# Optimization experiments

Hardware: AMD Instinct MI355X
Metric: run time of the kernel (lower is better)

Reference implementation:

```python
import jax, jax.numpy as jnp
import numpy as np

BINS = 6  # torch.histc(bins=6, min=0, max=256) in rarity()


def _border_mask(h, w, dtype):
    m = jnp.ones((h, w), dtype)
    return m.at[0, :].set(0).at[-1, :].set(0).at[:, 0].set(0).at[:, -1].set(0)


def _norm(x, lo, hi, axes):
    # normalize_tensor: map to [lo,hi]; all-zeros if constant map
    mn = x.min(axes, keepdims=True)
    mx = x.max(axes, keepdims=True)
    d = mx - mn
    ds = jnp.where(d == 0, jnp.ones_like(d), d)
    out = (x - mn) / ds * (hi - lo) + lo
    return jnp.where(d == 0, jnp.zeros_like(out), out)


def _ponder(x, axes):
    # map_ponderation: normalize to [0,1] then scale by (max-mean)^2
    w = (x.max(axes, keepdims=True) - x.mean(axes, keepdims=True)) ** 2
    return _norm(x, 0.0, 1.0, axes) * w


def _rarity_all(ch):
    # Vectorized rarity() over all channels. ch: [C,H,W]
    C, H, W = ch.shape
    ch = ch * _border_mask(H, W, ch.dtype)          # zero 1-px border
    ch = _norm(ch, 0.0, 256.0, (1, 2))              # per-channel -> [0,256]
    # torch.histc over [0,256]: bin = floor(v*bins/256), max value in last bin
    bin_idx = jnp.clip((ch * (BINS / 256.0)).astype(jnp.int32), 0, BINS - 1)
    hist = jax.nn.one_hot(bin_idx, BINS, dtype=ch.dtype).sum((1, 2))  # [C,BINS]
    hist = hist / hist.sum(-1, keepdims=True)
    hist = -jnp.log(hist + 1e-4)
    # lookup: (channel*bins - 1).long().clamp(0, bins-1)  (channel in [0,256], as in source)
    lut_idx = jnp.clip((ch * BINS - 1).astype(jnp.int32), 0, BINS - 1)
    dst = hist[jnp.arange(C)[:, None, None], lut_idx]  # [C,H,W] rarity lookup
    dst = _norm(dst, 0.0, 1.0, (1, 2))
    return _ponder(dst, (1, 2))


def _apply_rarity(x):
    # x: [1,C,H,W] -> [H,W]
    ch = x[0]
    H, W = ch.shape[-2:]
    r = _rarity_all(ch)
    # channel 0: ponderated again, no extra border zeroing (as in source)
    p0 = _ponder(r[0], (0, 1))
    rest = r[1:] * _border_mask(H, W, r.dtype)  # channels 1..C-1: border zeroed
    p = p0 + _ponder(rest, (1, 2)).sum(0)
    return _norm(p, 0.0, 1.0, (0, 1))  # threshold=None -> no thresholding


def _resize240(m):
    # T.Resize((240,240), bilinear) ~ half-pixel linear resize
    return jax.image.resize(m, (240, 240), method='linear')


def _forward(layers):
    # group layers into packs by spatial resolution (static, shapes known)
    packs = {}
    for t in layers:
        packs.setdefault(t.shape[-2:], []).append(t)
    group_maps = []
    for pack in packs.values():
        maps = [_resize240(_apply_rarity(t)) for t in pack]
        fused = maps[0] * 0.0
        for m in maps:  # fuse_itti
            fused = fused + _ponder(m, (0, 1))
        group_maps.append(_norm(fused, 0.0, 256.0, (0, 1)))
    groups = jnp.stack(group_maps, -1)  # [240,240,n_packs]
    return groups.sum(-1), groups


def setup_inputs() -> dict:
    key = jax.random.key(0)
    shapes = ([(1, 64, 224, 224)] * 2 + [(1, 128, 112, 112)] * 2 +
              [(1, 256, 56, 56)] * 3 + [(1, 512, 28, 28)] * 3 +
              [(1, 512, 14, 14)] * 3)
    keys = jax.random.split(key, len(shapes))
    return {f"x{i}": jax.random.uniform(keys[i], s, jnp.float32)
            for i, s in enumerate(shapes)}


def reference(x0, x1, x2, x3, x4, x5, x6, x7, x8, x9, x10, x11, x12):
    return _forward([x0, x1, x2, x3, x4, x5, x6, x7, x8, x9, x10, x11, x12])
```

## Files before the change

kernel.cpp:

```cpp
#include <hip/hip_runtime.h>
#include <math.h>

#define NT 13
#define RHW 57600
#define PIXB 8192

struct Meta {
  const float* x[NT];
  int C[NT];
  int H[NT];
  float hsc[NT];
  int chanOff[NT + 1];
  int pixOff[NT + 1];
  int mmOff[NT + 1];
  int nchMM[NT];
  int pmOff[NT + 1];
  int npcPM[NT];
  int pcOff[NT + 1];
};

__device__ __forceinline__ unsigned encf(float f) {
  unsigned u = __float_as_uint(f);
  return (u & 0x80000000u) ? ~u : (u | 0x80000000u);
}
__device__ __forceinline__ float decf(unsigned e) {
  unsigned u = (e & 0x80000000u) ? (e & 0x7fffffffu) : ~e;
  return __uint_as_float(u);
}

__device__ __forceinline__ int segOf(const int* off, int b) {
  int t = 0;
  while (t + 1 < NT && b >= off[t + 1]) t++;
  return t;
}

__global__ __launch_bounds__(256) void k_init(unsigned* cstats, unsigned* hist,
                                              unsigned long long* pq, int co, int po) {
  int i = blockIdx.x * 256 + threadIdx.x;
  int stride = gridDim.x * 256;
  for (int k = i; k < po; k += stride) pq[k] = 0ull;
  for (int k = i; k < 12 * co; k += stride) hist[k] = 0u;
  for (int k = i; k < co; k += stride) { cstats[2 * k] = 0xFFFFFFFFu; cstats[2 * k + 1] = 0u; }
}

template <int HH>
__device__ __forceinline__ void mm_body(const float* __restrict__ ch, int pix0, int pix1, float& mn, float& mx) {
  constexpr int W = HH, H = HH;
  int i40 = pix0 >> 2, i41 = pix1 >> 2;
  for (int i4 = i40 + (int)threadIdx.x; i4 < i41; i4 += 256) {
    float4 v = reinterpret_cast<const float4*>(ch)[i4];
#pragma unroll
    for (int j = 0; j < 4; j++) {
      int idx = i4 * 4 + j;
      int h = idx / W, w = idx - h * W;
      bool ok = h > 0 && h < (H - 1) && w > 0 && w < (W - 1);
      float f = (j == 0) ? v.x : (j == 1) ? v.y : (j == 2) ? v.z : v.w;
      if (ok) { mn = fminf(mn, f); mx = fmaxf(mx, f); }
    }
  }
}

__global__ __launch_bounds__(256) void k_minmax(Meta m, unsigned* cstats) {
  int b = blockIdx.x;
  int t = segOf(m.mmOff, b);
  int local = b - m.mmOff[t];
  int nch = m.nchMM[t];
  int c = local / nch, k = local - c * nch;
  int HW = m.H[t] * m.H[t];
  const float* ch = m.x[t] + (size_t)c * HW;
  int pix0 = k * PIXB, pix1 = min(pix0 + PIXB, HW);
  float mn = INFINITY, mx = -INFINITY;
  switch (m.H[t]) {
    case 224: mm_body<224>(ch, pix0, pix1, mn, mx); break;
    case 112: mm_body<112>(ch, pix0, pix1, mn, mx); break;
    case 56:  mm_body<56>(ch, pix0, pix1, mn, mx); break;
    case 28:  mm_body<28>(ch, pix0, pix1, mn, mx); break;
    default:  mm_body<14>(ch, pix0, pix1, mn, mx); break;
  }
#pragma unroll
  for (int o = 32; o > 0; o >>= 1) {
    mn = fminf(mn, __shfl_down(mn, o));
    mx = fmaxf(mx, __shfl_down(mx, o));
  }
  __shared__ float smn[4], smx[4];
  int wid = threadIdx.x >> 6;
  if ((threadIdx.x & 63) == 0) { smn[wid] = mn; smx[wid] = mx; }
  __syncthreads();
  if (threadIdx.x == 0) {
    for (int i = 1; i < 4; i++) { mn = fminf(mn, smn[i]); mx = fmaxf(mx, smx[i]); }
    int g = m.chanOff[t] + c;
    atomicMin(&cstats[2 * g], encf(mn));
    atomicMax(&cstats[2 * g + 1], encf(mx));
  }
}

template <int HH>
__device__ __forceinline__ void hist_body(const float* __restrict__ ch, int pix0, int pix1,
                                          float mn, float invd, unsigned* sh) {
  constexpr int W = HH, H = HH;
  int i40 = pix0 >> 2, i41 = pix1 >> 2;
  int nIter = (i41 - i40 + 255) >> 8;
  int lane = threadIdx.x & 63;
  unsigned cnt = 0;
  for (int it = 0; it < nIter; ++it) {
    int i4 = i40 + it * 256 + (int)threadIdx.x;
    bool valid = i4 < i41;
    float4 v = make_float4(0.f, 0.f, 0.f, 0.f);
    if (valid) v = reinterpret_cast<const float4*>(ch)[i4];
    int code[8];
#pragma unroll
    for (int j = 0; j < 4; j++) {
      int idx = i4 * 4 + j;
      int h = idx / W, w = idx - h * W;
      bool ok = valid && h > 0 && h < (H - 1) && w > 0 && w < (W - 1);
      float f = (j == 0) ? v.x : (j == 1) ? v.y : (j == 2) ? v.z : v.w;
      float vv = (f - mn) * invd * 256.0f;
      int bin = (int)(vv * 0.0234375f);
      bin = bin < 0 ? 0 : (bin > 5 ? 5 : bin);
      float tt = vv * 6.0f - 1.0f;
      int li = (int)tt;
      li = li < 0 ? 0 : (li > 5 ? 5 : li);
      code[j] = ok ? bin : -1;
      code[4 + j] = ok ? li : -1;
    }
#pragma unroll
    for (int j = 0; j < 4; j++) {
#pragma unroll
      for (int q = 0; q < 6; q++) {
        unsigned long long mb = __ballot(code[j] == q);
        if (lane == q) cnt += (unsigned)__popcll(mb);
        unsigned long long ml = __ballot(code[4 + j] == q);
        if (lane == 6 + q) cnt += (unsigned)__popcll(ml);
      }
    }
  }
  if (lane < 12) atomicAdd(&sh[lane], cnt);
}

__global__ __launch_bounds__(256) void k_hist(Meta m, const unsigned* cstats, unsigned* hist) {
  int b = blockIdx.x;
  int t = segOf(m.mmOff, b);
  int local = b - m.mmOff[t];
  int nch = m.nchMM[t];
  int c = local / nch, k = local - c * nch;
  int HW = m.H[t] * m.H[t];
  const float* ch = m.x[t] + (size_t)c * HW;
  int g = m.chanOff[t] + c;
  float mn = fminf(decf(cstats[2 * g]), 0.f);
  float mx = fmaxf(decf(cstats[2 * g + 1]), 0.f);
  float d = mx - mn;
  float invd = d > 0.f ? 1.0f / d : 0.f;
  int pix0 = k * PIXB, pix1 = min(pix0 + PIXB, HW);
  __shared__ unsigned sh[12];
  if (threadIdx.x < 12) sh[threadIdx.x] = 0;
  __syncthreads();
  switch (m.H[t]) {
    case 224: hist_body<224>(ch, pix0, pix1, mn, invd, sh); break;
    case 112: hist_body<112>(ch, pix0, pix1, mn, invd, sh); break;
    case 56:  hist_body<56>(ch, pix0, pix1, mn, invd, sh); break;
    case 28:  hist_body<28>(ch, pix0, pix1, mn, invd, sh); break;
    default:  hist_body<14>(ch, pix0, pix1, mn, invd, sh); break;
  }
  __syncthreads();
  if (threadIdx.x < 12) atomicAdd(&hist[12 * g + threadIdx.x], sh[threadIdx.x]);
}

__global__ void k_lut(Meta m, const unsigned* cstats, const unsigned* hist, float* lutg, int nch) {
  int b = blockIdx.x * blockDim.x + threadIdx.x;
  if (b >= nch) return;
  int t = segOf(m.chanOff, b);
  int cl = b - m.chanOff[t];
  int H = m.H[t], W = m.H[t], HW = H * W;
  float fHW = (float)HW;
  int nb = 2 * (H + W) - 4;
  float mn = fminf(decf(cstats[2 * b]), 0.f);
  float mx = fmaxf(decf(cstats[2 * b + 1]), 0.f);
  float d = mx - mn;
  float invd = d > 0.f ? 1.0f / d : 0.f;
  float vb = (0.f - mn) * invd * 256.0f;
  int bin_b = (int)(vb * 0.0234375f);
  bin_b = bin_b < 0 ? 0 : (bin_b > 5 ? 5 : bin_b);
  float ttb = vb * 6.0f - 1.0f;
  int lib = (int)ttb;
  lib = lib < 0 ? 0 : (lib > 5 ? 5 : lib);
  unsigned hh[12];
  for (int j = 0; j < 12; j++) hh[j] = hist[12 * b + j];
  hh[bin_b] += (unsigned)nb;
  hh[6 + lib] += (unsigned)nb;
  float hl[6];
  for (int j = 0; j < 6; j++) hl[j] = -logf((float)hh[j] / fHW + 1e-4f);
  float mn2 = INFINITY, mx2 = -INFINITY, sum2 = 0.f;
  for (int j = 0; j < 6; j++) {
    unsigned cc = hh[6 + j];
    if (cc) { mn2 = fminf(mn2, hl[j]); mx2 = fmaxf(mx2, hl[j]); sum2 += (float)cc * hl[j]; }
  }
  float d2 = mx2 - mn2;
  float RL[6];
  if (d2 > 0.f) {
    float meanN = (sum2 / fHW - mn2) / d2;
    float w = 1.0f - meanN; w *= w;
    for (int j = 0; j < 6; j++) RL[j] = (hl[j] - mn2) / d2 * w;
  } else {
    for (int j = 0; j < 6; j++) RL[j] = 0.f;
  }
  float LUT[7];
  if (cl == 0) {
    float mnr = INFINITY, mxr = -INFINITY, sumr = 0.f;
    for (int j = 0; j < 6; j++) {
      unsigned cc = hh[6 + j];
      if (cc) { mnr = fminf(mnr, RL[j]); mxr = fmaxf(mxr, RL[j]); sumr += (float)cc * RL[j]; }
    }
    float dr = mxr - mnr;
    if (dr > 0.f) {
      float meanr = sumr / fHW;
      float wp = mxr - meanr; wp *= wp;
      for (int j = 0; j < 6; j++) LUT[j] = (RL[j] - mnr) / dr * wp;
      LUT[6] = LUT[lib];
    } else {
      for (int j = 0; j < 7; j++) LUT[j] = 0.f;
    }
  } else {
    float mnr = 0.f, mxr = 0.f, sumr = 0.f;
    for (int j = 0; j < 6; j++) {
      int cc = (int)hh[6 + j] - (j == lib ? nb : 0);
      if (cc > 0) { mnr = fminf(mnr, RL[j]); mxr = fmaxf(mxr, RL[j]); sumr += (float)cc * RL[j]; }
    }
    float dr = mxr - mnr;
    if (dr > 0.f) {
      float meanr = sumr / fHW;
      float wp = mxr - meanr; wp *= wp;
      for (int j = 0; j < 6; j++) LUT[j] = (RL[j] - mnr) / dr * wp;
      LUT[6] = (0.f - mnr) / dr * wp;
    } else {
      for (int j = 0; j < 7; j++) LUT[j] = 0.f;
    }
  }
  float* o = lutg + (size_t)b * 9;
  for (int j = 0; j < 7; j++) o[j] = LUT[j];
  o[7] = mn; o[8] = invd;
}

#define CCH 32
template <int HH>
__device__ __forceinline__ void pm_body(const float* __restrict__ X, int cbase, int ncb, int i4lo, int i4hi,
                                        const float* sLut, const float* sMn, const float* sInv,
                                        unsigned long long* __restrict__ Q) {
  constexpr int W = HH, H = HH;
  constexpr int HW = H * W;
  int i4 = i4lo + (int)threadIdx.x;
  if (i4 >= i4hi) return;
  int base = i4 * 4;
  int b0, b1, b2, b3;
  { int idx = base + 0; int h = idx / W, w = idx - h * W; b0 = (h == 0 || h == H - 1 || w == 0 || w == W - 1); }
  { int idx = base + 1; int h = idx / W, w = idx - h * W; b1 = (h == 0 || h == H - 1 || w == 0 || w == W - 1); }
  { int idx = base + 2; int h = idx / W, w = idx - h * W; b2 = (h == 0 || h == H - 1 || w == 0 || w == W - 1); }
  { int idx = base + 3; int h = idx / W, w = idx - h * W; b3 = (h == 0 || h == H - 1 || w == 0 || w == W - 1); }
  float a0 = 0.f, a1 = 0.f, a2 = 0.f, a3 = 0.f;
  const float4* Xp = reinterpret_cast<const float4*>(X + (size_t)cbase * HW);
#pragma unroll 4
  for (int cl = 0; cl < ncb; ++cl) {
    float4 v = Xp[(size_t)cl * (HW / 4) + i4];
    float mnc = sMn[cl], ivc = sInv[cl];
    const float* L = sLut + cl * 8;
    { float vv = (v.x - mnc) * ivc * 256.0f; float tt = vv * 6.0f - 1.0f; int li = (int)tt; li = li < 0 ? 0 : (li > 5 ? 5 : li); a0 += L[b0 ? 6 : li]; }
    { float vv = (v.y - mnc) * ivc * 256.0f; float tt = vv * 6.0f - 1.0f; int li = (int)tt; li = li < 0 ? 0 : (li > 5 ? 5 : li); a1 += L[b1 ? 6 : li]; }
    { float vv = (v.z - mnc) * ivc * 256.0f; float tt = vv * 6.0f - 1.0f; int li = (int)tt; li = li < 0 ? 0 : (li > 5 ? 5 : li); a2 += L[b2 ? 6 : li]; }
    { float vv = (v.w - mnc) * ivc * 256.0f; float tt = vv * 6.0f - 1.0f; int li = (int)tt; li = li < 0 ? 0 : (li > 5 ? 5 : li); a3 += L[b3 ? 6 : li]; }
  }
  atomicAdd(&Q[base + 0], (unsigned long long)((double)a0 * 4294967296.0));
  atomicAdd(&Q[base + 1], (unsigned long long)((double)a1 * 4294967296.0));
  atomicAdd(&Q[base + 2], (unsigned long long)((double)a2 * 4294967296.0));
  atomicAdd(&Q[base + 3], (unsigned long long)((double)a3 * 4294967296.0));
}

__global__ __launch_bounds__(256) void k_pmapQ(Meta m, const float* lutg, unsigned long long* pmapsQ) {
  __shared__ float sLut[CCH * 8];
  __shared__ float sMn[CCH];
  __shared__ float sInv[CCH];
  int b = blockIdx.x;
  int t = segOf(m.pmOff, b);
  int local = b - m.pmOff[t];
  int npc = m.npcPM[t];
  int cc = local / npc, pc = local - cc * npc;
  int C = m.C[t], HW = m.H[t] * m.H[t];
  int cbase = cc * CCH;
  int ncb = min(CCH, C - cbase);
  for (int i = threadIdx.x; i < ncb; i += 256) {
    const float* L = lutg + (size_t)(m.chanOff[t] + cbase + i) * 9;
#pragma unroll
    for (int j = 0; j < 7; j++) sLut[i * 8 + j] = L[j];
    sLut[i * 8 + 7] = 0.f;
    sMn[i] = L[7]; sInv[i] = L[8];
  }
  __syncthreads();
  int i4lo = pc * 256;
  int i4hi = min(i4lo + 256, HW >> 2);
  unsigned long long* Q = pmapsQ + m.pixOff[t];
  switch (m.H[t]) {
    case 224: pm_body<224>(m.x[t], cbase, ncb, i4lo, i4hi, sLut, sMn, sInv, Q); break;
    case 112: pm_body<112>(m.x[t], cbase, ncb, i4lo, i4hi, sLut, sMn, sInv, Q); break;
    case 56:  pm_body<56>(m.x[t], cbase, ncb, i4lo, i4hi, sLut, sMn, sInv, Q); break;
    case 28:  pm_body<28>(m.x[t], cbase, ncb, i4lo, i4hi, sLut, sMn, sInv, Q); break;
    default:  pm_body<14>(m.x[t], cbase, ncb, i4lo, i4hi, sLut, sMn, sInv, Q); break;
  }
}

__global__ __launch_bounds__(256) void k_pconv(Meta m, const unsigned long long* pmapsQ, float* pmaps, float* ppart) {
  int b = blockIdx.x;
  int t = segOf(m.pcOff, b);
  int HW = m.H[t] * m.H[t];
  int chunk = b - m.pcOff[t];
  int i4 = chunk * 256 + (int)threadIdx.x;
  float mn = INFINITY, mx = -INFINITY;
  if (i4 < (HW >> 2)) {
    size_t off = (size_t)m.pixOff[t] + (size_t)i4 * 4;
    const double inv = 1.0 / 4294967296.0;
    float4 f;
    f.x = (float)((double)pmapsQ[off + 0] * inv);
    f.y = (float)((double)pmapsQ[off + 1] * inv);
    f.z = (float)((double)pmapsQ[off + 2] * inv);
    f.w = (float)((double)pmapsQ[off + 3] * inv);
    *reinterpret_cast<float4*>(pmaps + off) = f;
    mn = fminf(fminf(f.x, f.y), fminf(f.z, f.w));
    mx = fmaxf(fmaxf(f.x, f.y), fmaxf(f.z, f.w));
  }
#pragma unroll
  for (int o = 32; o > 0; o >>= 1) {
    mn = fminf(mn, __shfl_down(mn, o));
    mx = fmaxf(mx, __shfl_down(mx, o));
  }
  __shared__ float smn[4], smx[4];
  int wid = threadIdx.x >> 6;
  if ((threadIdx.x & 63) == 0) { smn[wid] = mn; smx[wid] = mx; }
  __syncthreads();
  if (threadIdx.x == 0) {
    for (int i = 1; i < 4; i++) { mn = fminf(mn, smn[i]); mx = fmaxf(mx, smx[i]); }
    ppart[2 * b] = mn; ppart[2 * b + 1] = mx;
  }
}

__global__ __launch_bounds__(256) void k_resize(Meta m, const float* pmaps, const float* ppart,
                                                float* mmaps, float* rpart) {
  __shared__ float sMnT, sInvT;
  int t = blockIdx.x / 225;
  int blk = blockIdx.x % 225;
  int wid = threadIdx.x >> 6, lane = threadIdx.x & 63;
  if (wid == 0) {
    int n = m.pcOff[t + 1] - m.pcOff[t];
    const float* pp = ppart + (size_t)m.pcOff[t] * 2;
    float mn = INFINITY, mx = -INFINITY;
    if (lane < n) { mn = pp[2 * lane]; mx = pp[2 * lane + 1]; }
#pragma unroll
    for (int o = 32; o > 0; o >>= 1) {
      mn = fminf(mn, __shfl_down(mn, o));
      mx = fmaxf(mx, __shfl_down(mx, o));
    }
    if (lane == 0) {
      float d = mx - mn;
      sMnT = mn; sInvT = d > 0.f ? 1.0f / d : 0.f;
    }
  }
  __syncthreads();
  int pix = blk * 256 + threadIdx.x;
  int H = m.H[t], W = m.H[t];
  const float* p = pmaps + m.pixOff[t];
  float mn = sMnT, a = sInvT;
  int oy = pix / 240, ox = pix - oy * 240;
  float hs = m.hsc[t];
  float sy = ((float)oy + 0.5f) * hs - 0.5f;
  float sx = ((float)ox + 0.5f) * hs - 0.5f;
  float fy0 = floorf(sy), fx0 = floorf(sx);
  float fy = sy - fy0, fx = sx - fx0;
  int iy0 = (int)fy0, ix0 = (int)fx0;
  int y0 = iy0 < 0 ? 0 : (iy0 > H - 1 ? H - 1 : iy0);
  int y1 = iy0 + 1 < 0 ? 0 : (iy0 + 1 > H - 1 ? H - 1 : iy0 + 1);
  int x0 = ix0 < 0 ? 0 : (ix0 > W - 1 ? W - 1 : ix0);
  int x1 = ix0 + 1 < 0 ? 0 : (ix0 + 1 > W - 1 ? W - 1 : ix0 + 1);
  float v00 = p[y0 * W + x0], v01 = p[y0 * W + x1];
  float v10 = p[y1 * W + x0], v11 = p[y1 * W + x1];
  float r = (1.f - fy) * ((1.f - fx) * v00 + fx * v01) + fy * ((1.f - fx) * v10 + fx * v11);
  float mv = (r - mn) * a;
  mmaps[(size_t)t * RHW + pix] = mv;
  float bmn = mv, bmx = mv, bsm = mv;
#pragma unroll
  for (int o = 32; o > 0; o >>= 1) {
    bmn = fminf(bmn, __shfl_down(bmn, o));
    bmx = fmaxf(bmx, __shfl_down(bmx, o));
    bsm += __shfl_down(bsm, o);
  }
  __shared__ float smn[4], smx[4], ssm[4];
  if ((threadIdx.x & 63) == 0) { smn[wid] = bmn; smx[wid] = bmx; ssm[wid] = bsm; }
  __syncthreads();
  if (threadIdx.x == 0) {
    for (int i = 1; i < 4; i++) { bmn = fminf(bmn, smn[i]); bmx = fmaxf(bmx, smx[i]); bsm += ssm[i]; }
    float* rp = rpart + ((size_t)t * 225 + blk) * 3;
    rp[0] = bmn; rp[1] = bmx; rp[2] = bsm;
  }
}

__global__ __launch_bounds__(256) void k_fuse(const float* mmaps, const float* rpart,
                                              float* fusedm, float* fpart) {
  __shared__ float sMn[3], sD[3], sW[3];
  int g = blockIdx.x / 225;
  int blk = blockIdx.x % 225;
  const int gs[6] = {0, 2, 4, 7, 10, 13};
  int nt = gs[g + 1] - gs[g];
  int wid = threadIdx.x >> 6, lane = threadIdx.x & 63;
  if (wid < nt) {
    int t = gs[g] + wid;
    const float* rp = rpart + (size_t)t * 225 * 3;
    float mn = INFINITY, mx = -INFINITY, sm = 0.f;
    for (int i = lane; i < 225; i += 64) {
      mn = fminf(mn, rp[3 * i]); mx = fmaxf(mx, rp[3 * i + 1]); sm += rp[3 * i + 2];
    }
#pragma unroll
    for (int o = 32; o > 0; o >>= 1) {
      mn = fminf(mn, __shfl_down(mn, o));
      mx = fmaxf(mx, __shfl_down(mx, o));
      sm += __shfl_down(sm, o);
    }
    if (lane == 0) {
      float d = mx - mn;
      if (d > 0.f) {
        float mean = sm * (1.0f / 57600.0f);
        float w = mx - mean; w *= w;
        sMn[wid] = mn; sD[wid] = d; sW[wid] = w;
      } else {
        sMn[wid] = 0.f; sD[wid] = 0.f; sW[wid] = 0.f;
      }
    }
  }
  __syncthreads();
  int pix = blk * 256 + threadIdx.x;
  float acc = 0.f;
  for (int k = 0; k < nt; k++) {
    int t = gs[g] + k;
    if (sD[k] > 0.f) acc += (mmaps[(size_t)t * RHW + pix] - sMn[k]) / sD[k] * sW[k];
  }
  fusedm[(size_t)g * RHW + pix] = acc;
  float bmn = acc, bmx = acc;
#pragma unroll
  for (int o = 32; o > 0; o >>= 1) {
    bmn = fminf(bmn, __shfl_down(bmn, o));
    bmx = fmaxf(bmx, __shfl_down(bmx, o));
  }
  __shared__ float smn[4], smx[4];
  if ((threadIdx.x & 63) == 0) { smn[wid] = bmn; smx[wid] = bmx; }
  __syncthreads();
  if (threadIdx.x == 0) {
    for (int i = 1; i < 4; i++) { bmn = fminf(bmn, smn[i]); bmx = fmaxf(bmx, smx[i]); }
    float* fp = fpart + ((size_t)g * 225 + blk) * 2;
    fp[0] = bmn; fp[1] = bmx;
  }
}

__global__ __launch_bounds__(256) void k_out(const float* fusedm, const float* fpart, float* out) {
  __shared__ float fmn[5], finv[5];
  int wid = threadIdx.x >> 6, lane = threadIdx.x & 63;
  for (int g = wid; g < 5; g += 4) {
    const float* fp = fpart + (size_t)g * 225 * 2;
    float mn = INFINITY, mx = -INFINITY;
    for (int i = lane; i < 225; i += 64) {
      mn = fminf(mn, fp[2 * i]); mx = fmaxf(mx, fp[2 * i + 1]);
    }
#pragma unroll
    for (int o = 32; o > 0; o >>= 1) {
      mn = fminf(mn, __shfl_down(mn, o));
      mx = fmaxf(mx, __shfl_down(mx, o));
    }
    if (lane == 0) {
      float d = mx - mn;
      fmn[g] = mn; finv[g] = d > 0.f ? 256.0f / d : 0.f;
    }
  }
  __syncthreads();
  int pix = blockIdx.x * 256 + threadIdx.x;
  float acc = 0.f;
  float* out2 = out + RHW;
#pragma unroll
  for (int g = 0; g < 5; g++) {
    float v = (fusedm[(size_t)g * RHW + pix] - fmn[g]) * finv[g];
    out2[(size_t)pix * 5 + g] = v;
    acc += v;
  }
  out[pix] = acc;
}

extern "C" void kernel_launch(void* const* d_in, const int* in_sizes, int n_in,
                              void* d_out, int out_size, void* d_ws, size_t ws_size,
                              hipStream_t stream) {
  static const int Cs[NT] = {64, 64, 128, 128, 256, 256, 256, 512, 512, 512, 512, 512, 512};
  static const int Hs[NT] = {224, 224, 112, 112, 56, 56, 56, 28, 28, 28, 14, 14, 14};
  Meta m;
  int co = 0, po = 0, mmb = 0, pmb = 0, pcb = 0;
  for (int t = 0; t < NT; t++) {
    m.x[t] = (const float*)d_in[t];
    m.C[t] = Cs[t]; m.H[t] = Hs[t];
    m.hsc[t] = (float)((double)Hs[t] / 240.0);
    int HW = Hs[t] * Hs[t];
    m.chanOff[t] = co; co += Cs[t];
    m.pixOff[t] = po; po += HW;
    m.mmOff[t] = mmb;
    m.nchMM[t] = (HW + PIXB - 1) / PIXB;
    mmb += Cs[t] * m.nchMM[t];
    m.pmOff[t] = pmb;
    m.npcPM[t] = (HW + 1023) / 1024;
    pmb += m.npcPM[t] * ((Cs[t] + CCH - 1) / CCH);
    m.pcOff[t] = pcb;
    pcb += (HW + 1023) / 1024;
  }
  m.chanOff[NT] = co; m.pixOff[NT] = po; m.mmOff[NT] = mmb; m.pmOff[NT] = pmb; m.pcOff[NT] = pcb;

  size_t off = 0;
  auto a16 = [](size_t x) { return (x + 15) & ~(size_t)15; };
#define WALLOC(var, type, count) type* var = (type*)((char*)d_ws + off); off = a16(off + sizeof(type) * (size_t)(count));
  WALLOC(cstats, unsigned, 2 * co)
  WALLOC(hist, unsigned, 12 * co)
  WALLOC(lutg, float, 9 * co)
  WALLOC(ppart, float, 2 * pcb)
  WALLOC(rpart, float, NT * 225 * 3)
  WALLOC(fpart, float, 5 * 225 * 2)
  WALLOC(pmaps, float, po)
  WALLOC(mmaps, float, NT * RHW)
  WALLOC(fusedm, float, 5 * RHW)
#undef WALLOC
  unsigned long long* pmapsQ = (unsigned long long*)mmaps;

  hipLaunchKernelGGL(k_init, dim3(512), dim3(256), 0, stream, cstats, hist, pmapsQ, co, po);
  hipLaunchKernelGGL(k_minmax, dim3(mmb), dim3(256), 0, stream, m, cstats);
  hipLaunchKernelGGL(k_hist, dim3(mmb), dim3(256), 0, stream, m, cstats, hist);
  hipLaunchKernelGGL(k_lut, dim3((co + 255) / 256), dim3(256), 0, stream, m, cstats, hist, lutg, co);
  hipLaunchKernelGGL(k_pmapQ, dim3(pmb), dim3(256), 0, stream, m, lutg, pmapsQ);
  hipLaunchKernelGGL(k_pconv, dim3(pcb), dim3(256), 0, stream, m, pmapsQ, pmaps, ppart);
  hipLaunchKernelGGL(k_resize, dim3(NT * 225), dim3(256), 0, stream, m, pmaps, ppart, mmaps, rpart);
  hipLaunchKernelGGL(k_fuse, dim3(5 * 225), dim3(256), 0, stream, mmaps, rpart, fusedm, fpart);
  hipLaunchKernelGGL(k_out, dim3(225), dim3(256), 0, stream, fusedm, fpart, (float*)d_out);
}
```

Baseline: 91.14 us.

## Remove atomics: per-block partials, fused LUT+pmap kernel with in-block channel reduction

Replaces global atomic min/max and histogram accumulation with per-block partial arrays that consumers reduce, which drops the init kernel. The histogram now counts into packed 10-bit register fields plus wave shuffles instead of 48 ballots per float4. The LUT computation is folded into a new k_pmap kernel. That kernel reduces all channels for a 256-pixel tile inside one 512-thread block through shared memory, replacing the 64-bit fixed-point atomics and the separate conversion kernel. In exchange, LUT math is recomputed redundantly in every pmap block, and occupancy drops because of the large shared-memory footprint.

Result: faster. 77.44 us (-15.0%).

```diff
diff --git a/kernel.cpp b/kernel.cpp
--- a/kernel.cpp
+++ b/kernel.cpp
@@ -10,37 +10,16 @@
   int C[NT];
   int H[NT];
   float hsc[NT];
-  int chanOff[NT + 1];
   int pixOff[NT + 1];
   int mmOff[NT + 1];
   int nchMM[NT];
   int pmOff[NT + 1];
-  int npcPM[NT];
-  int pcOff[NT + 1];
 };
-
-__device__ __forceinline__ unsigned encf(float f) {
-  unsigned u = __float_as_uint(f);
-  return (u & 0x80000000u) ? ~u : (u | 0x80000000u);
-}
-__device__ __forceinline__ float decf(unsigned e) {
-  unsigned u = (e & 0x80000000u) ? (e & 0x7fffffffu) : ~e;
-  return __uint_as_float(u);
-}
 
 __device__ __forceinline__ int segOf(const int* off, int b) {
   int t = 0;
   while (t + 1 < NT && b >= off[t + 1]) t++;
   return t;
-}
-
-__global__ __launch_bounds__(256) void k_init(unsigned* cstats, unsigned* hist,
-                                              unsigned long long* pq, int co, int po) {
-  int i = blockIdx.x * 256 + threadIdx.x;
-  int stride = gridDim.x * 256;
-  for (int k = i; k < po; k += stride) pq[k] = 0ull;
-  for (int k = i; k < 12 * co; k += stride) hist[k] = 0u;
-  for (int k = i; k < co; k += stride) { cstats[2 * k] = 0xFFFFFFFFu; cstats[2 * k + 1] = 0u; }
 }
 
 template <int HH>
@@ -60,7 +39,7 @@
   }
 }
 
-__global__ __launch_bounds__(256) void k_minmax(Meta m, unsigned* cstats) {
+__global__ __launch_bounds__(256) void k_minmax(Meta m, float* cpart) {
   int b = blockIdx.x;
   int t = segOf(m.mmOff, b);
   int local = b - m.mmOff[t];
@@ -88,26 +67,22 @@
   __syncthreads();
   if (threadIdx.x == 0) {
     for (int i = 1; i < 4; i++) { mn = fminf(mn, smn[i]); mx = fmaxf(mx, smx[i]); }
-    int g = m.chanOff[t] + c;
-    atomicMin(&cstats[2 * g], encf(mn));
-    atomicMax(&cstats[2 * g + 1], encf(mx));
+    cpart[2 * b] = mn; cpart[2 * b + 1] = mx;
   }
 }
 
 template <int HH>
 __device__ __forceinline__ void hist_body(const float* __restrict__ ch, int pix0, int pix1,
-                                          float mn, float invd, unsigned* sh) {
+                                          float mn, float invd,
+                                          unsigned long long& cbin, unsigned long long& clut) {
   constexpr int W = HH, H = HH;
   int i40 = pix0 >> 2, i41 = pix1 >> 2;
   int nIter = (i41 - i40 + 255) >> 8;
-  int lane = threadIdx.x & 63;
-  unsigned cnt = 0;
   for (int it = 0; it < nIter; ++it) {
     int i4 = i40 + it * 256 + (int)threadIdx.x;
     bool valid = i4 < i41;
     float4 v = make_float4(0.f, 0.f, 0.f, 0.f);
     if (valid) v = reinterpret_cast<const float4*>(ch)[i4];
-    int code[8];
 #pragma unroll
     for (int j = 0; j < 4; j++) {
       int idx = i4 * 4 + j;
@@ -120,24 +95,13 @@
       float tt = vv * 6.0f - 1.0f;
       int li = (int)tt;
       li = li < 0 ? 0 : (li > 5 ? 5 : li);
-      code[j] = ok ? bin : -1;
-      code[4 + j] = ok ? li : -1;
-    }
-#pragma unroll
-    for (int j = 0; j < 4; j++) {
-#pragma unroll
-      for (int q = 0; q < 6; q++) {
-        unsigned long long mb = __ballot(code[j] == q);
-        if (lane == q) cnt += (unsigned)__popcll(mb);
-        unsigned long long ml = __ballot(code[4 + j] == q);
-        if (lane == 6 + q) cnt += (unsigned)__popcll(ml);
-      }
-    }
-  }
-  if (lane < 12) atomicAdd(&sh[lane], cnt);
-}
-
-__global__ __launch_bounds__(256) void k_hist(Meta m, const unsigned* cstats, unsigned* hist) {
+      cbin += (unsigned long long)ok << (bin * 10);
+      clut += (unsigned long long)ok << (li * 10);
+    }
+  }
+}
+
+__global__ __launch_bounds__(256) void k_hist(Meta m, const float* cpart, unsigned* hpart) {
   int b = blockIdx.x;
   int t = segOf(m.mmOff, b);
   int local = b - m.mmOff[t];
@@ -145,197 +109,209 @@
   int c = local / nch, k = local - c * nch;
   int HW = m.H[t] * m.H[t];
   const float* ch = m.x[t] + (size_t)c * HW;
-  int g = m.chanOff[t] + c;
-  float mn = fminf(decf(cstats[2 * g]), 0.f);
-  float mx = fmaxf(decf(cstats[2 * g + 1]), 0.f);
+  int cb = m.mmOff[t] + c * nch;
+  float mn = INFINITY, mx = -INFINITY;
+  for (int kk = 0; kk < nch; kk++) {
+    mn = fminf(mn, cpart[2 * (cb + kk)]);
+    mx = fmaxf(mx, cpart[2 * (cb + kk) + 1]);
+  }
+  mn = fminf(mn, 0.f);
+  mx = fmaxf(mx, 0.f);
   float d = mx - mn;
   float invd = d > 0.f ? 1.0f / d : 0.f;
   int pix0 = k * PIXB, pix1 = min(pix0 + PIXB, HW);
-  __shared__ unsigned sh[12];
-  if (threadIdx.x < 12) sh[threadIdx.x] = 0;
-  __syncthreads();
+  unsigned long long cbin = 0ull, clut = 0ull;
   switch (m.H[t]) {
-    case 224: hist_body<224>(ch, pix0, pix1, mn, invd, sh); break;
-    case 112: hist_body<112>(ch, pix0, pix1, mn, invd, sh); break;
-    case 56:  hist_body<56>(ch, pix0, pix1, mn, invd, sh); break;
-    case 28:  hist_body<28>(ch, pix0, pix1, mn, invd, sh); break;
-    default:  hist_body<14>(ch, pix0, pix1, mn, invd, sh); break;
-  }
-  __syncthreads();
-  if (threadIdx.x < 12) atomicAdd(&hist[12 * g + threadIdx.x], sh[threadIdx.x]);
-}
-
-__global__ void k_lut(Meta m, const unsigned* cstats, const unsigned* hist, float* lutg, int nch) {
-  int b = blockIdx.x * blockDim.x + threadIdx.x;
-  if (b >= nch) return;
-  int t = segOf(m.chanOff, b);
-  int cl = b - m.chanOff[t];
-  int H = m.H[t], W = m.H[t], HW = H * W;
-  float fHW = (float)HW;
-  int nb = 2 * (H + W) - 4;
-  float mn = fminf(decf(cstats[2 * b]), 0.f);
-  float mx = fmaxf(decf(cstats[2 * b + 1]), 0.f);
-  float d = mx - mn;
-  float invd = d > 0.f ? 1.0f / d : 0.f;
-  float vb = (0.f - mn) * invd * 256.0f;
-  int bin_b = (int)(vb * 0.0234375f);
-  bin_b = bin_b < 0 ? 0 : (bin_b > 5 ? 5 : bin_b);
-  float ttb = vb * 6.0f - 1.0f;
-  int lib = (int)ttb;
-  lib = lib < 0 ? 0 : (lib > 5 ? 5 : lib);
-  unsigned hh[12];
-  for (int j = 0; j < 12; j++) hh[j] = hist[12 * b + j];
-  hh[bin_b] += (unsigned)nb;
-  hh[6 + lib] += (unsigned)nb;
-  float hl[6];
-  for (int j = 0; j < 6; j++) hl[j] = -logf((float)hh[j] / fHW + 1e-4f);
-  float mn2 = INFINITY, mx2 = -INFINITY, sum2 = 0.f;
-  for (int j = 0; j < 6; j++) {
-    unsigned cc = hh[6 + j];
-    if (cc) { mn2 = fminf(mn2, hl[j]); mx2 = fmaxf(mx2, hl[j]); sum2 += (float)cc * hl[j]; }
-  }
-  float d2 = mx2 - mn2;
-  float RL[6];
-  if (d2 > 0.f) {
-    float meanN = (sum2 / fHW - mn2) / d2;
-    float w = 1.0f - meanN; w *= w;
-    for (int j = 0; j < 6; j++) RL[j] = (hl[j] - mn2) / d2 * w;
-  } else {
-    for (int j = 0; j < 6; j++) RL[j] = 0.f;
-  }
-  float LUT[7];
-  if (cl == 0) {
-    float mnr = INFINITY, mxr = -INFINITY, sumr = 0.f;
+    case 224: hist_body<224>(ch, pix0, pix1, mn, invd, cbin, clut); break;
+    case 112: hist_body<112>(ch, pix0, pix1, mn, invd, cbin, clut); break;
+    case 56:  hist_body<56>(ch, pix0, pix1, mn, invd, cbin, clut); break;
+    case 28:  hist_body<28>(ch, pix0, pix1, mn, invd, cbin, clut); break;
+    default:  hist_body<14>(ch, pix0, pix1, mn, invd, cbin, clut); break;
+  }
+  unsigned pk[6];
+#pragma unroll
+  for (int j = 0; j < 6; j++)
+    pk[j] = (unsigned)((cbin >> (10 * j)) & 1023ull) | ((unsigned)((clut >> (10 * j)) & 1023ull) << 16);
+#pragma unroll
+  for (int o = 32; o > 0; o >>= 1) {
+#pragma unroll
+    for (int j = 0; j < 6; j++) pk[j] += __shfl_down(pk[j], o);
+  }
+  __shared__ unsigned swh[4][12];
+  int wid = threadIdx.x >> 6, lane = threadIdx.x & 63;
+  if (lane == 0) {
+#pragma unroll
+    for (int j = 0; j < 6; j++) { swh[wid][j] = pk[j] & 0xffffu; swh[wid][6 + j] = pk[j] >> 16; }
+  }
+  __syncthreads();
+  if (threadIdx.x < 12)
+    hpart[12 * b + threadIdx.x] =
+        swh[0][threadIdx.x] + swh[1][threadIdx.x] + swh[2][threadIdx.x] + swh[3][threadIdx.x];
+}
+
+template <int HH>
+__device__ __forceinline__ void pm_inner(const float* __restrict__ X, int i4, bool act,
+                                         int c0, int c1, const float* sLut,
+                                         const float* sMn, const float* sInv, float* a) {
+  constexpr int W = HH, H = HH;
+  constexpr int i4n = (H * W) / 4;
+  if (!act) return;
+  int bf[4];
+#pragma unroll
+  for (int j = 0; j < 4; j++) {
+    int idx = i4 * 4 + j;
+    int h = idx / W, w = idx - h * W;
+    bf[j] = (h == 0 || h == H - 1 || w == 0 || w == W - 1) ? 1 : 0;
+  }
+  const float4* Xp = reinterpret_cast<const float4*>(X);
+#pragma unroll 4
+  for (int c = c0; c < c1; ++c) {
+    float4 v = Xp[(size_t)c * i4n + i4];
+    float mnc = sMn[c], ivc = sInv[c];
+    const float* L = sLut + c * 8;
+    float fv0 = v.x, fv1 = v.y, fv2 = v.z, fv3 = v.w;
+    { float vv = (fv0 - mnc) * ivc * 256.0f; float tt = vv * 6.0f - 1.0f; int li = (int)tt; li = li < 0 ? 0 : (li > 5 ? 5 : li); a[0] += L[bf[0] ? 6 : li]; }
+    { float vv = (fv1 - mnc) * ivc * 256.0f; float tt = vv * 6.0f - 1.0f; int li = (int)tt; li = li < 0 ? 0 : (li > 5 ? 5 : li); a[1] += L[bf[1] ? 6 : li]; }
+    { float vv = (fv2 - mnc) * ivc * 256.0f; float tt = vv * 6.0f - 1.0f; int li = (int)tt; li = li < 0 ? 0 : (li > 5 ? 5 : li); a[2] += L[bf[2] ? 6 : li]; }
+    { float vv = (fv3 - mnc) * ivc * 256.0f; float tt = vv * 6.0f - 1.0f; int li = (int)tt; li = li < 0 ? 0 : (li > 5 ? 5 : li); a[3] += L[bf[3] ? 6 : li]; }
+  }
+}
+
+__global__ __launch_bounds__(512) void k_pmap(Meta m, const float* cpart, const unsigned* hpart,
+                                              float* pmaps, float* ppart) {
+  __shared__ float sLut[512 * 8];
+  __shared__ float sMn[512], sInv[512];
+  __shared__ float sAcc[8][256];
+  int b = blockIdx.x;
+  int t = segOf(m.pmOff, b);
+  int blk = b - m.pmOff[t];
+  int C = m.C[t], H = m.H[t], W = H, HW = H * W;
+  int nch = m.nchMM[t];
+  int tid = threadIdx.x;
+  if (tid < C) {
+    int cb = m.mmOff[t] + tid * nch;
+    float mn = INFINITY, mx = -INFINITY;
+    unsigned hh[12];
+#pragma unroll
+    for (int j = 0; j < 12; j++) hh[j] = 0u;
+    for (int k = 0; k < nch; k++) {
+      mn = fminf(mn, cpart[2 * (cb + k)]);
+      mx = fmaxf(mx, cpart[2 * (cb + k) + 1]);
+#pragma unroll
+      for (int j = 0; j < 12; j++) hh[j] += hpart[12 * (cb + k) + j];
+    }
+    mn = fminf(mn, 0.f); mx = fmaxf(mx, 0.f);
+    float d = mx - mn;
+    float invd = d > 0.f ? 1.0f / d : 0.f;
+    float fHW = (float)HW;
+    int nb = 2 * (H + W) - 4;
+    float vb = (0.f - mn) * invd * 256.0f;
+    int bin_b = (int)(vb * 0.0234375f);
+    bin_b = bin_b < 0 ? 0 : (bin_b > 5 ? 5 : bin_b);
+    float ttb = vb * 6.0f - 1.0f;
+    int lib = (int)ttb;
+    lib = lib < 0 ? 0 : (lib > 5 ? 5 : lib);
+    hh[bin_b] += (unsigned)nb;
+    hh[6 + lib] += (unsigned)nb;
+    float hl[6];
+#pragma unroll
+    for (int j = 0; j < 6; j++) hl[j] = -logf((float)hh[j] / fHW + 1e-4f);
+    float mn2 = INFINITY, mx2 = -INFINITY, sum2 = 0.f;
+#pragma unroll
     for (int j = 0; j < 6; j++) {
       unsigned cc = hh[6 + j];
-      if (cc) { mnr = fminf(mnr, RL[j]); mxr = fmaxf(mxr, RL[j]); sumr += (float)cc * RL[j]; }
-    }
-    float dr = mxr - mnr;
-    if (dr > 0.f) {
-      float meanr = sumr / fHW;
-      float wp = mxr - meanr; wp *= wp;
-      for (int j = 0; j < 6; j++) LUT[j] = (RL[j] - mnr) / dr * wp;
-      LUT[6] = LUT[lib];
+      if (cc) { mn2 = fminf(mn2, hl[j]); mx2 = fmaxf(mx2, hl[j]); sum2 += (float)cc * hl[j]; }
+    }
+    float d2 = mx2 - mn2;
+    float RL[6];
+    if (d2 > 0.f) {
+      float meanN = (sum2 / fHW - mn2) / d2;
+      float w = 1.0f - meanN; w *= w;
+#pragma unroll
+      for (int j = 0; j < 6; j++) RL[j] = (hl[j] - mn2) / d2 * w;
     } else {
-      for (int j = 0; j < 7; j++) LUT[j] = 0.f;
-    }
-  } else {
-    float mnr = 0.f, mxr = 0.f, sumr = 0.f;
-    for (int j = 0; j < 6; j++) {
-      int cc = (int)hh[6 + j] - (j == lib ? nb : 0);
-      if (cc > 0) { mnr = fminf(mnr, RL[j]); mxr = fmaxf(mxr, RL[j]); sumr += (float)cc * RL[j]; }
-    }
-    float dr = mxr - mnr;
-    if (dr > 0.f) {
-      float meanr = sumr / fHW;
-      float wp = mxr - meanr; wp *= wp;
-      for (int j = 0; j < 6; j++) LUT[j] = (RL[j] - mnr) / dr * wp;
-      LUT[6] = (0.f - mnr) / dr * wp;
+#pragma unroll
+      for (int j = 0; j < 6; j++) RL[j] = 0.f;
+    }
+    float LUT[7];
+    if (tid == 0) {
+      float mnr = INFINITY, mxr = -INFINITY, sumr = 0.f;
+#pragma unroll
+      for (int j = 0; j < 6; j++) {
+        unsigned cc = hh[6 + j];
+        if (cc) { mnr = fminf(mnr, RL[j]); mxr = fmaxf(mxr, RL[j]); sumr += (float)cc * RL[j]; }
+      }
+      float dr = mxr - mnr;
+      if (dr > 0.f) {
+        float meanr = sumr / fHW;
+        float wp = mxr - meanr; wp *= wp;
+#pragma unroll
+        for (int j = 0; j < 6; j++) LUT[j] = (RL[j] - mnr) / dr * wp;
+        LUT[6] = LUT[lib];
+      } else {
+#pragma unroll
+        for (int j = 0; j < 7; j++) LUT[j] = 0.f;
+      }
     } else {
-      for (int j = 0; j < 7; j++) LUT[j] = 0.f;
-    }
-  }
-  float* o = lutg + (size_t)b * 9;
-  for (int j = 0; j < 7; j++) o[j] = LUT[j];
-  o[7] = mn; o[8] = invd;
-}
-
-#define CCH 32
-template <int HH>
-__device__ __forceinline__ void pm_body(const float* __restrict__ X, int cbase, int ncb, int i4lo, int i4hi,
-                                        const float* sLut, const float* sMn, const float* sInv,
-                                        unsigned long long* __restrict__ Q) {
-  constexpr int W = HH, H = HH;
-  constexpr int HW = H * W;
-  int i4 = i4lo + (int)threadIdx.x;
-  if (i4 >= i4hi) return;
-  int base = i4 * 4;
-  int b0, b1, b2, b3;
-  { int idx = base + 0; int h = idx / W, w = idx - h * W; b0 = (h == 0 || h == H - 1 || w == 0 || w == W - 1); }
-  { int idx = base + 1; int h = idx / W, w = idx - h * W; b1 = (h == 0 || h == H - 1 || w == 0 || w == W - 1); }
-  { int idx = base + 2; int h = idx / W, w = idx - h * W; b2 = (h == 0 || h == H - 1 || w == 0 || w == W - 1); }
-  { int idx = base + 3; int h = idx / W, w = idx - h * W; b3 = (h == 0 || h == H - 1 || w == 0 || w == W - 1); }
-  float a0 = 0.f, a1 = 0.f, a2 = 0.f, a3 = 0.f;
-  const float4* Xp = reinterpret_cast<const float4*>(X + (size_t)cbase * HW);
-#pragma unroll 4
-  for (int cl = 0; cl < ncb; ++cl) {
-    float4 v = Xp[(size_t)cl * (HW / 4) + i4];
-    float mnc = sMn[cl], ivc = sInv[cl];
-    const float* L = sLut + cl * 8;
-    { float vv = (v.x - mnc) * ivc * 256.0f; float tt = vv * 6.0f - 1.0f; int li = (int)tt; li = li < 0 ? 0 : (li > 5 ? 5 : li); a0 += L[b0 ? 6 : li]; }
-    { float vv = (v.y - mnc) * ivc * 256.0f; float tt = vv * 6.0f - 1.0f; int li = (int)tt; li = li < 0 ? 0 : (li > 5 ? 5 : li); a1 += L[b1 ? 6 : li]; }
-    { float vv = (v.z - mnc) * ivc * 256.0f; float tt = vv * 6.0f - 1.0f; int li = (int)tt; li = li < 0 ? 0 : (li > 5 ? 5 : li); a2 += L[b2 ? 6 : li]; }
-    { float vv = (v.w - mnc) * ivc * 256.0f; float tt = vv * 6.0f - 1.0f; int li = (int)tt; li = li < 0 ? 0 : (li > 5 ? 5 : li); a3 += L[b3 ? 6 : li]; }
-  }
-  atomicAdd(&Q[base + 0], (unsigned long long)((double)a0 * 4294967296.0));
-  atomicAdd(&Q[base + 1], (unsigned long long)((double)a1 * 4294967296.0));
-  atomicAdd(&Q[base + 2], (unsigned long long)((double)a2 * 4294967296.0));
-  atomicAdd(&Q[base + 3], (unsigned long long)((double)a3 * 4294967296.0));
-}
-
-__global__ __launch_bounds__(256) void k_pmapQ(Meta m, const float* lutg, unsigned long long* pmapsQ) {
-  __shared__ float sLut[CCH * 8];
-  __shared__ float sMn[CCH];
-  __shared__ float sInv[CCH];
-  int b = blockIdx.x;
-  int t = segOf(m.pmOff, b);
-  int local = b - m.pmOff[t];
-  int npc = m.npcPM[t];
-  int cc = local / npc, pc = local - cc * npc;
-  int C = m.C[t], HW = m.H[t] * m.H[t];
-  int cbase = cc * CCH;
-  int ncb = min(CCH, C - cbase);
-  for (int i = threadIdx.x; i < ncb; i += 256) {
-    const float* L = lutg + (size_t)(m.chanOff[t] + cbase + i) * 9;
-#pragma unroll
-    for (int j = 0; j < 7; j++) sLut[i * 8 + j] = L[j];
-    sLut[i * 8 + 7] = 0.f;
-    sMn[i] = L[7]; sInv[i] = L[8];
-  }
-  __syncthreads();
-  int i4lo = pc * 256;
-  int i4hi = min(i4lo + 256, HW >> 2);
-  unsigned long long* Q = pmapsQ + m.pixOff[t];
-  switch (m.H[t]) {
-    case 224: pm_body<224>(m.x[t], cbase, ncb, i4lo, i4hi, sLut, sMn, sInv, Q); break;
-    case 112: pm_body<112>(m.x[t], cbase, ncb, i4lo, i4hi, sLut, sMn, sInv, Q); break;
-    case 56:  pm_body<56>(m.x[t], cbase, ncb, i4lo, i4hi, sLut, sMn, sInv, Q); break;
-    case 28:  pm_body<28>(m.x[t], cbase, ncb, i4lo, i4hi, sLut, sMn, sInv, Q); break;
-    default:  pm_body<14>(m.x[t], cbase, ncb, i4lo, i4hi, sLut, sMn, sInv, Q); break;
-  }
-}
-
-__global__ __launch_bounds__(256) void k_pconv(Meta m, const unsigned long long* pmapsQ, float* pmaps, float* ppart) {
-  int b = blockIdx.x;
-  int t = segOf(m.pcOff, b);
-  int HW = m.H[t] * m.H[t];
-  int chunk = b - m.pcOff[t];
-  int i4 = chunk * 256 + (int)threadIdx.x;
-  float mn = INFINITY, mx = -INFINITY;
-  if (i4 < (HW >> 2)) {
-    size_t off = (size_t)m.pixOff[t] + (size_t)i4 * 4;
-    const double inv = 1.0 / 4294967296.0;
-    float4 f;
-    f.x = (float)((double)pmapsQ[off + 0] * inv);
-    f.y = (float)((double)pmapsQ[off + 1] * inv);
-    f.z = (float)((double)pmapsQ[off + 2] * inv);
-    f.w = (float)((double)pmapsQ[off + 3] * inv);
-    *reinterpret_cast<float4*>(pmaps + off) = f;
-    mn = fminf(fminf(f.x, f.y), fminf(f.z, f.w));
-    mx = fmaxf(fmaxf(f.x, f.y), fmaxf(f.z, f.w));
-  }
-#pragma unroll
-  for (int o = 32; o > 0; o >>= 1) {
-    mn = fminf(mn, __shfl_down(mn, o));
-    mx = fmaxf(mx, __shfl_down(mx, o));
-  }
-  __shared__ float smn[4], smx[4];
-  int wid = threadIdx.x >> 6;
-  if ((threadIdx.x & 63) == 0) { smn[wid] = mn; smx[wid] = mx; }
-  __syncthreads();
-  if (threadIdx.x == 0) {
-    for (int i = 1; i < 4; i++) { mn = fminf(mn, smn[i]); mx = fmaxf(mx, smx[i]); }
-    ppart[2 * b] = mn; ppart[2 * b + 1] = mx;
+      float mnr = 0.f, mxr = 0.f, sumr = 0.f;
+#pragma unroll
+      for (int j = 0; j < 6; j++) {
+        int cc = (int)hh[6 + j] - (j == lib ? nb : 0);
+        if (cc > 0) { mnr = fminf(mnr, RL[j]); mxr = fmaxf(mxr, RL[j]); sumr += (float)cc * RL[j]; }
+      }
+      float dr = mxr - mnr;
+      if (dr > 0.f) {
+        float meanr = sumr / fHW;
+        float wp = mxr - meanr; wp *= wp;
+#pragma unroll
+        for (int j = 0; j < 6; j++) LUT[j] = (RL[j] - mnr) / dr * wp;
+        LUT[6] = (0.f - mnr) / dr * wp;
+      } else {
+#pragma unroll
+        for (int j = 0; j < 7; j++) LUT[j] = 0.f;
+      }
+    }
+#pragma unroll
+    for (int j = 0; j < 7; j++) sLut[tid * 8 + j] = LUT[j];
+    sLut[tid * 8 + 7] = 0.f;
+    sMn[tid] = mn; sInv[tid] = invd;
+  }
+  __syncthreads();
+  int wid = tid >> 6, lane = tid & 63;
+  int i4n = HW >> 2;
+  int i4 = blk * 64 + lane;
+  bool act = i4 < i4n;
+  float a[4] = {0.f, 0.f, 0.f, 0.f};
+  int cpw = C >> 3;
+  switch (H) {
+    case 224: pm_inner<224>(m.x[t], i4, act, wid * cpw, (wid + 1) * cpw, sLut, sMn, sInv, a); break;
+    case 112: pm_inner<112>(m.x[t], i4, act, wid * cpw, (wid + 1) * cpw, sLut, sMn, sInv, a); break;
+    case 56:  pm_inner<56>(m.x[t], i4, act, wid * cpw, (wid + 1) * cpw, sLut, sMn, sInv, a); break;
+    case 28:  pm_inner<28>(m.x[t], i4, act, wid * cpw, (wid + 1) * cpw, sLut, sMn, sInv, a); break;
+    default:  pm_inner<14>(m.x[t], i4, act, wid * cpw, (wid + 1) * cpw, sLut, sMn, sInv, a); break;
+  }
+  *reinterpret_cast<float4*>(&sAcc[wid][lane * 4]) = make_float4(a[0], a[1], a[2], a[3]);
+  __syncthreads();
+  if (wid == 0) {
+    float bmn = INFINITY, bmx = -INFINITY;
+    if (act) {
+      float t0 = 0.f, t1 = 0.f, t2 = 0.f, t3 = 0.f;
+#pragma unroll
+      for (int w = 0; w < 8; w++) {
+        const float* s = &sAcc[w][lane * 4];
+        t0 += s[0]; t1 += s[1]; t2 += s[2]; t3 += s[3];
+      }
+      size_t o = (size_t)m.pixOff[t] + (size_t)i4 * 4;
+      *reinterpret_cast<float4*>(pmaps + o) = make_float4(t0, t1, t2, t3);
+      bmn = fminf(fminf(t0, t1), fminf(t2, t3));
+      bmx = fmaxf(fmaxf(t0, t1), fmaxf(t2, t3));
+    }
+#pragma unroll
+    for (int o = 32; o > 0; o >>= 1) {
+      bmn = fminf(bmn, __shfl_down(bmn, o));
+      bmx = fmaxf(bmx, __shfl_down(bmx, o));
+    }
+    if (lane == 0) { ppart[2 * b] = bmn; ppart[2 * b + 1] = bmx; }
   }
 }
 
@@ -346,10 +322,10 @@
   int blk = blockIdx.x % 225;
   int wid = threadIdx.x >> 6, lane = threadIdx.x & 63;
   if (wid == 0) {
-    int n = m.pcOff[t + 1] - m.pcOff[t];
-    const float* pp = ppart + (size_t)m.pcOff[t] * 2;
+    int n = m.pmOff[t + 1] - m.pmOff[t];
+    const float* pp = ppart + (size_t)m.pmOff[t] * 2;
     float mn = INFINITY, mx = -INFINITY;
-    if (lane < n) { mn = pp[2 * lane]; mx = pp[2 * lane + 1]; }
+    for (int i = lane; i < n; i += 64) { mn = fminf(mn, pp[2 * i]); mx = fmaxf(mx, pp[2 * i + 1]); }
 #pragma unroll
     for (int o = 32; o > 0; o >>= 1) {
       mn = fminf(mn, __shfl_down(mn, o));
@@ -492,46 +468,37 @@
   static const int Cs[NT] = {64, 64, 128, 128, 256, 256, 256, 512, 512, 512, 512, 512, 512};
   static const int Hs[NT] = {224, 224, 112, 112, 56, 56, 56, 28, 28, 28, 14, 14, 14};
   Meta m;
-  int co = 0, po = 0, mmb = 0, pmb = 0, pcb = 0;
+  int po = 0, mmb = 0, pmb = 0;
   for (int t = 0; t < NT; t++) {
     m.x[t] = (const float*)d_in[t];
     m.C[t] = Cs[t]; m.H[t] = Hs[t];
     m.hsc[t] = (float)((double)Hs[t] / 240.0);
     int HW = Hs[t] * Hs[t];
-    m.chanOff[t] = co; co += Cs[t];
     m.pixOff[t] = po; po += HW;
     m.mmOff[t] = mmb;
     m.nchMM[t] = (HW + PIXB - 1) / PIXB;
     mmb += Cs[t] * m.nchMM[t];
     m.pmOff[t] = pmb;
-    m.npcPM[t] = (HW + 1023) / 1024;
-    pmb += m.npcPM[t] * ((Cs[t] + CCH - 1) / CCH);
-    m.pcOff[t] = pcb;
-    pcb += (HW + 1023) / 1024;
-  }
-  m.chanOff[NT] = co; m.pixOff[NT] = po; m.mmOff[NT] = mmb; m.pmOff[NT] = pmb; m.pcOff[NT] = pcb;
+    pmb += (HW + 255) / 256;
+  }
+  m.pixOff[NT] = po; m.mmOff[NT] = mmb; m.pmOff[NT] = pmb;
 
   size_t off = 0;
   auto a16 = [](size_t x) { return (x + 15) & ~(size_t)15; };
 #define WALLOC(var, type, count) type* var = (type*)((char*)d_ws + off); off = a16(off + sizeof(type) * (size_t)(count));
-  WALLOC(cstats, unsigned, 2 * co)
-  WALLOC(hist, unsigned, 12 * co)
-  WALLOC(lutg, float, 9 * co)
-  WALLOC(ppart, float, 2 * pcb)
+  WALLOC(cpart, float, 2 * mmb)
+  WALLOC(hpart, unsigned, 12 * mmb)
+  WALLOC(ppart, float, 2 * pmb)
   WALLOC(rpart, float, NT * 225 * 3)
   WALLOC(fpart, float, 5 * 225 * 2)
   WALLOC(pmaps, float, po)
   WALLOC(mmaps, float, NT * RHW)
   WALLOC(fusedm, float, 5 * RHW)
 #undef WALLOC
-  unsigned long long* pmapsQ = (unsigned long long*)mmaps;
-
-  hipLaunchKernelGGL(k_init, dim3(512), dim3(256), 0, stream, cstats, hist, pmapsQ, co, po);
-  hipLaunchKernelGGL(k_minmax, dim3(mmb), dim3(256), 0, stream, m, cstats);
-  hipLaunchKernelGGL(k_hist, dim3(mmb), dim3(256), 0, stream, m, cstats, hist);
-  hipLaunchKernelGGL(k_lut, dim3((co + 255) / 256), dim3(256), 0, stream, m, cstats, hist, lutg, co);
-  hipLaunchKernelGGL(k_pmapQ, dim3(pmb), dim3(256), 0, stream, m, lutg, pmapsQ);
-  hipLaunchKernelGGL(k_pconv, dim3(pcb), dim3(256), 0, stream, m, pmapsQ, pmaps, ppart);
+
+  hipLaunchKernelGGL(k_minmax, dim3(mmb), dim3(256), 0, stream, m, cpart);
+  hipLaunchKernelGGL(k_hist, dim3(mmb), dim3(256), 0, stream, m, cpart, hpart);
+  hipLaunchKernelGGL(k_pmap, dim3(pmb), dim3(512), 0, stream, m, cpart, hpart, pmaps, ppart);
   hipLaunchKernelGGL(k_resize, dim3(NT * 225), dim3(256), 0, stream, m, pmaps, ppart, mmaps, rpart);
   hipLaunchKernelGGL(k_fuse, dim3(5 * 225), dim3(256), 0, stream, mmaps, rpart, fusedm, fpart);
   hipLaunchKernelGGL(k_out, dim3(225), dim3(256), 0, stream, fusedm, fpart, (float*)d_out);
```
